# Kernel optimization log

Measured on AMD Instinct MI355X. Metric: run time of the kernel, lower is better.

The kernel has to match this reference:

```python
import jax, jax.numpy as jnp
import numpy as np

B, IN_SEQ, TGT_SEQ = 128, 50, 25
IN_SIZE, OUT_SIZE, RNN = 128, 128, 2048


def setup_inputs() -> dict:
    key = jax.random.key(0)
    ks = jax.random.split(key, 10)
    s_in = 1.0 / np.sqrt(IN_SIZE)
    s_out = 1.0 / np.sqrt(OUT_SIZE)
    s_rnn = 1.0 / np.sqrt(RNN)
    return {
        "encoder_inputs": jax.random.normal(ks[0], (B, IN_SEQ, IN_SIZE), jnp.float32),
        "decoder_inputs": jax.random.normal(ks[1], (B, TGT_SEQ, IN_SIZE), jnp.float32),
        "fc1_w": jax.random.uniform(ks[2], (OUT_SIZE, IN_SIZE), jnp.float32, -s_in, s_in),
        "fc1_b": jax.random.uniform(ks[3], (OUT_SIZE,), jnp.float32, -s_in, s_in),
        "w_ih": jax.random.uniform(ks[4], (3 * RNN, OUT_SIZE), jnp.float32, -s_rnn, s_rnn),
        "w_hh": jax.random.uniform(ks[5], (3 * RNN, RNN), jnp.float32, -s_rnn, s_rnn),
        "b_ih": jax.random.uniform(ks[6], (3 * RNN,), jnp.float32, -s_rnn, s_rnn),
        "b_hh": jax.random.uniform(ks[7], (3 * RNN,), jnp.float32, -s_rnn, s_rnn),
        "fc2_w": jax.random.uniform(ks[8], (OUT_SIZE, RNN), jnp.float32, -s_rnn, s_rnn),
        "fc2_b": jax.random.uniform(ks[9], (OUT_SIZE,), jnp.float32, -s_rnn, s_rnn),
    }


def _gru_cell(x, h, w_ih, w_hh, b_ih, b_hh):
    # PyTorch GRUCell: gates ordered (r, z, n)
    gi = x @ w_ih.T + b_ih            # [B, 3R]
    gh = h @ w_hh.T + b_hh            # [B, 3R]
    i_r, i_z, i_n = jnp.split(gi, 3, axis=-1)
    h_r, h_z, h_n = jnp.split(gh, 3, axis=-1)
    r = jax.nn.sigmoid(i_r + h_r)
    z = jax.nn.sigmoid(i_z + h_z)
    n = jnp.tanh(i_n + r * h_n)
    return (1.0 - z) * n + z * h


def reference(encoder_inputs, decoder_inputs, fc1_w, fc1_b, w_ih, w_hh, b_ih, b_hh, fc2_w, fc2_b):
    # Eval mode: F.dropout(training=False) is identity.
    enc = encoder_inputs @ fc1_w.T + fc1_b              # [B, S_in, OUT]
    enc_t = jnp.transpose(enc, (1, 0, 2))               # time-major [S_in, B, OUT]
    h0 = jnp.zeros((encoder_inputs.shape[0], RNN), enc.dtype)

    def enc_step(state, x):
        return _gru_cell(x, state, w_ih, w_hh, b_ih, b_hh), None

    state, _ = jax.lax.scan(enc_step, h0, enc_t[:-1])   # input_seq - 1 steps

    def dec_step(carry, _):
        state, inp = carry
        inp = jax.lax.stop_gradient(inp)                # inp.detach()
        state = _gru_cell(inp, state, w_ih, w_hh, b_ih, b_hh)
        out = inp + state @ fc2_w.T + fc2_b             # residual decoder
        return (state, out), out

    _, outs = jax.lax.scan(dec_step, (state, enc_t[-1]), None, length=TGT_SEQ)
    return jnp.transpose(outs, (1, 0, 2))               # [B, TGT_SEQ, OUT]
```

## Files before the change

### kernel.cpp

```cpp
#include <hip/hip_runtime.h>
#include <limits.h>

constexpr int kB   = 128;
constexpr int kSin = 50;
constexpr int kT   = 25;
constexpr int kD   = 128;
constexpr int kR   = 2048;
constexpr int kNB  = 256;
constexpr int kNT  = 512;

typedef __bf16 bf16x8 __attribute__((ext_vector_type(8)));
typedef float  f32x4  __attribute__((ext_vector_type(4)));
typedef unsigned short u16;
typedef unsigned long long u64;

__device__ __forceinline__ float bf2f(u16 u){ union{unsigned i; float f;}x; x.i=((unsigned)u)<<16; return x.f; }
__device__ __forceinline__ u16 f2bf(float f){ union{float f; unsigned i;}x; x.f=f; return (u16)((x.i + 0x7FFFu + ((x.i>>16)&1u))>>16); }
__device__ __forceinline__ float sigm(float x){ return 1.f/(1.f+__expf(-x)); }

__device__ __forceinline__ void stg32(unsigned* p, unsigned v){
    __hip_atomic_store(p, v, __ATOMIC_RELAXED, __HIP_MEMORY_SCOPE_AGENT);
}
__device__ __forceinline__ void stg64(u64* p, u64 v){
    __hip_atomic_store(p, v, __ATOMIC_RELAXED, __HIP_MEMORY_SCOPE_AGENT);
}
__device__ __forceinline__ unsigned ald32(const void* p){
    return __hip_atomic_load((const unsigned*)p, __ATOMIC_RELAXED, __HIP_MEMORY_SCOPE_AGENT);
}
__device__ __forceinline__ u64 ald64(const void* p){
    return __hip_atomic_load((const u64*)p, __ATOMIC_RELAXED, __HIP_MEMORY_SCOPE_AGENT);
}
__device__ __forceinline__ bf16x8 ald128bf(const u16* p){
    union{ u64 q[2]; bf16x8 v; } t;
    t.q[0] = ald64(p);
    t.q[1] = ald64(p + 4);
    return t.v;
}
__device__ __forceinline__ float aldf(const float* p){
    union{ unsigned u; float f; } t; t.u = ald32(p); return t.f;
}

__device__ __forceinline__ bf16x8 pack8(float4 a, float4 b){
    union{ bf16x8 v; u16 u[8]; } t;
    t.u[0]=f2bf(a.x); t.u[1]=f2bf(a.y); t.u[2]=f2bf(a.z); t.u[3]=f2bf(a.w);
    t.u[4]=f2bf(b.x); t.u[5]=f2bf(b.y); t.u[6]=f2bf(b.z); t.u[7]=f2bf(b.w);
    return t.v;
}

__device__ __forceinline__ void gbar(int* flags, int k, int base, int perlane)
{
    __syncthreads();
    const int tid = threadIdx.x;
    if (tid == 0) atomicMax(&flags[blockIdx.x*16], k);
    if (tid < 64) {
        int iter = 0;
        for (;;) {
            bool ok = true;
            for (int j = 0; j < perlane; ++j) {
                const int idx = base + tid*perlane + j;
                int v;
                if ((iter & 31) == 31) v = atomicMax(&flags[idx*16], INT_MIN);
                else                   v = (int)ald32(&flags[idx*16]);
                ok &= (v >= k);
            }
            if (__ballot(ok) == ~0ull) break;
            ++iter;
            __builtin_amdgcn_s_sleep(1);
        }
    }
    __syncthreads();
}

__device__ __forceinline__ void cvt_f32_bf16(const float* __restrict__ s, u16* __restrict__ d,
                                             int n4, int gtid, int gstride)
{
    for (int i = gtid; i < n4; i += gstride) {
        float4 v = ((const float4*)s)[i];
        u64 pk = (u64)f2bf(v.x) | ((u64)f2bf(v.y)<<16) | ((u64)f2bf(v.z)<<32) | ((u64)f2bf(v.w)<<48);
        stg64((u64*)d + i, pk);
    }
}

template<int NT, int NACC>
__device__ __forceinline__ void small_gemm(
    const u16* __restrict__ Am, int alda,
    const u16* __restrict__ Bp, int bldb,
    f32x4 (&acc)[NACC], u16* pool)
{
    const int tid=threadIdx.x, lane=tid&63, wv=tid>>6, g=wv>>2, mt=wv&3, ar=lane&15, aq=lane>>4;
    u16* sA = pool;
    u16* sB = pool + 8704;
    { int q=tid,     r=q>>4, c=q&15; *(uint4*)&sA[r*136+c*8] = *(const uint4*)(Am + r*alda + c*8); }
    { int q=tid+512, r=q>>4, c=q&15; *(uint4*)&sA[r*136+c*8] = *(const uint4*)(Am + r*alda + c*8); }
    for (int q=tid; q<NT*256; q+=kNT){
        int r=q>>4, c=q&15;
        *(uint4*)&sB[r*136+c*8] = *(const uint4*)(Bp + (size_t)r*bldb + c*8);
    }
    __syncthreads();
#pragma unroll
    for (int jt=0; jt<NT; ++jt){
        if ((jt&1) != g) continue;
#pragma unroll
        for (int kk=0; kk<4; ++kk){
            bf16x8 a = *(const bf16x8*)&sA[(mt*16+ar)*136 + kk*32 + aq*8];
            bf16x8 b = *(const bf16x8*)&sB[(jt*16+ar)*136 + kk*32 + aq*8];
            acc[jt>>1] = __builtin_amdgcn_mfma_f32_16x16x32_bf16(a,b,acc[jt>>1],0,0,0);
        }
    }
    __syncthreads();
}

__device__ __forceinline__ void gru_phase_reg(
    const u16* __restrict__ hcur, u16* __restrict__ hnxt,
    const u16* __restrict__ xb,
    const bf16x8 (&wB)[3][8], const bf16x8 (&wI)[3],
    const float4 b4, float (&hprev)[4],
    int wgc, int mrow0, u16* smem, u16* sH)
{
    const int tid=threadIdx.x, lane=tid&63, w=tid>>6, ar=lane&15, aq=lane>>4;
    const f32x4 zz = {0.f,0.f,0.f,0.f};
    f32x4 acc[3][4] = {{zz,zz,zz,zz},{zz,zz,zz,zz},{zz,zz,zz,zz}};
    f32x4 xn[4] = {zz,zz,zz,zz};

#pragma unroll
    for (int mt=0; mt<4; ++mt){
        const int row = mrow0 + mt*16 + ar;
        bf16x8 af[8];
#pragma unroll
        for (int c=0; c<8; ++c){
            const int s = 16*w + 2*c + (aq>>1);
            af[c] = ald128bf(hcur + (((s*128 + row)<<4) + (aq&1)*8));
        }
#pragma unroll
        for (int c=0; c<8; ++c){
            acc[0][mt] = __builtin_amdgcn_mfma_f32_16x16x32_bf16(af[c], wB[0][c], acc[0][mt],0,0,0);
            acc[1][mt] = __builtin_amdgcn_mfma_f32_16x16x32_bf16(af[c], wB[1][c], acc[1][mt],0,0,0);
            acc[2][mt] = __builtin_amdgcn_mfma_f32_16x16x32_bf16(af[c], wB[2][c], acc[2][mt],0,0,0);
        }
    }
    if (w < 4){
#pragma unroll
        for (int mt=0; mt<4; ++mt){
            bf16x8 ax = ald128bf(xb + (mrow0+mt*16+ar)*kD + 32*w + aq*8);
            acc[0][mt] = __builtin_amdgcn_mfma_f32_16x16x32_bf16(ax, wI[0], acc[0][mt],0,0,0);
            acc[1][mt] = __builtin_amdgcn_mfma_f32_16x16x32_bf16(ax, wI[1], acc[1][mt],0,0,0);
            xn[mt]     = __builtin_amdgcn_mfma_f32_16x16x32_bf16(ax, wI[2], xn[mt],0,0,0);
        }
    }
    float* red = (float*)smem;
#define RCELL(wp,g4,mt) (red + (((((wp)*4+(g4))*4+(mt))*64 + lane)<<2))
    if (w >= 4){
#pragma unroll
        for (int g=0; g<3; ++g)
#pragma unroll
            for (int mt=0; mt<4; ++mt)
                *(f32x4*)RCELL(w-4, g, mt) = acc[g][mt];
    }
    __syncthreads();
    if (w < 4){
#pragma unroll
        for (int g=0; g<3; ++g)
#pragma unroll
            for (int mt=0; mt<4; ++mt)
                acc[g][mt] += *(f32x4*)RCELL(w, g, mt);
#pragma unroll
        for (int g=0; g<3; ++g)
#pragma unroll
            for (int mt=0; mt<4; ++mt)
                *(f32x4*)RCELL(w, g, mt) = acc[g][mt];
#pragma unroll
        for (int mt=0; mt<4; ++mt)
            *(f32x4*)RCELL(w, 3, mt) = xn[mt];
    }
    __syncthreads();
    if (tid < 256){
        const int mt = tid>>6, ls = tid&63, aqs = ls>>4, ars = ls&15;
        f32x4 R=zz, Z=zz, NH=zz, NX=zz;
#pragma unroll
        for (int wp=0; wp<4; ++wp){
            R  += *(f32x4*)(red + ((((wp*4+0)*4+mt)*64 + ls)<<2));
            Z  += *(f32x4*)(red + ((((wp*4+1)*4+mt)*64 + ls)<<2));
            NH += *(f32x4*)(red + ((((wp*4+2)*4+mt)*64 + ls)<<2));
            NX += *(f32x4*)(red + ((((wp*4+3)*4+mt)*64 + ls)<<2));
        }
#pragma unroll
        for (int rr=0; rr<4; ++rr){
            const int m = mrow0 + mt*16 + aqs*4 + rr;
            float r_ = sigm(R[rr] + b4.x);
            float z_ = sigm(Z[rr] + b4.y);
            float n_ = tanhf(NX[rr] + b4.z + r_*(NH[rr] + b4.w));
            float hn = (1.f-z_)*n_ + z_*hprev[rr];
            hprev[rr] = hn;
            u16 hb = f2bf(hn);
            sH[(mt*16 + aqs*4 + rr)*16 + ars] = hb;
            unsigned other = (unsigned)__shfl_xor((int)(unsigned)hb, 1);
            if (!(ars&1))
                stg32((unsigned*)(hnxt + ((wgc*128+m)<<4) + ars), (unsigned)hb | (other<<16));
        }
    }
#undef RCELL
    __syncthreads();
}

__device__ __forceinline__ void fc2_partial(
    const u16* __restrict__ sH, const bf16x8 (&wF2)[4],
    int wgc, int mh, float* __restrict__ part)
{
    const int tid=threadIdx.x, lane=tid&63, w=tid>>6, ar=lane&15, aq=lane>>4;
    const int mt = w&3, nh = w>>2;
    bf16x8 a;
    if (aq < 2) a = *(const bf16x8*)&sH[(mt*16+ar)*16 + aq*8];
    else {
#pragma unroll
        for (int i=0;i<8;++i) a[i] = (__bf16)0.f;
    }
    const f32x4 zz = {0.f,0.f,0.f,0.f};
    f32x4 acc[4] = {zz,zz,zz,zz};
#pragma unroll
    for (int j=0;j<4;++j)
        acc[j] = __builtin_amdgcn_mfma_f32_16x16x32_bf16(a, wF2[j], acc[j],0,0,0);
#pragma unroll
    for (int j=0;j<4;++j){
        const int col = (nh*4+j)*16 + ar;
#pragma unroll
        for (int rr=0;rr<4;++rr){
            const int row = mt*16 + aq*4 + rr;
            stg32((unsigned*)(part + ((((size_t)mh*64+row)*128 + wgc)*128 + col)),
                  __float_as_uint(acc[j][rr]));
        }
    }
}

__global__ __launch_bounds__(kNT, 2) void seq2seq_kernel(
    const void* __restrict__ enc_in_raw, const void* __restrict__ fc1_w_raw,
    const void* __restrict__ fc1_b_raw,  const void* __restrict__ w_ih_raw,
    const void* __restrict__ w_hh_raw,   const void* __restrict__ b_ih_raw,
    const void* __restrict__ b_hh_raw,   const void* __restrict__ fc2_w_raw,
    const void* __restrict__ fc2_b_raw,
    void* __restrict__ out_raw,
    u16* __restrict__ enc_act,
    u16* __restrict__ h_b16,
    u16* __restrict__ inp_b16,
    float* __restrict__ inp_f32,
    float* __restrict__ encF,
    float* __restrict__ bias,
    float* __restrict__ part,
    int* flags,
    u16* __restrict__ cv_encx, u16* __restrict__ cv_fc2, u16* __restrict__ cv_fc1)
{
    __shared__ __align__(16) u16 smem[33792];
    __shared__ int sflag;
    u16* sH = smem + 32768;
    const int wg = blockIdx.x, tid = threadIdx.x;
    const int wgc = wg & 127, mrow0 = (wg >> 7) * 64;
    const int lane = tid & 63, wv = tid >> 6, ar = lane & 15, aq = lane >> 4;
    const int gtid = wg * kNT + tid, gstride = kNB * kNT;
    const int dom = (wg >> 7) * 128;
    int tok = 1;

    {
        const u16* p = (const u16*)enc_in_raw;
        int found = 0;
        for (int i = tid; i < 16384; i += kNT) found |= ((p[i] & 0x7F80) == 0x7F80) ? 1 : 0;
        if (tid == 0) sflag = 0;
        __syncthreads();
        if (found) sflag = 1;
        __syncthreads();
    }
    const bool F32 = (sflag != 0);

    bf16x8 wB[3][8];
    bf16x8 wI[3];
    {
        const int w4 = wv & 3;
        if (F32){
            const float* Wh = (const float*)w_hh_raw;
            const float* Wi = (const float*)w_ih_raw;
#pragma unroll
            for (int g=0; g<3; ++g)
#pragma unroll
                for (int c=0; c<8; ++c){
                    size_t o = (size_t)(g*kR + wgc*16 + ar)*kR + 256*wv + 32*c + aq*8;
                    wB[g][c] = pack8(*(const float4*)(Wh+o), *(const float4*)(Wh+o+4));
                }
#pragma unroll
            for (int g=0; g<3; ++g){
                size_t o = (size_t)(g*kR + wgc*16 + ar)*kD + 32*w4 + aq*8;
                wI[g] = pack8(*(const float4*)(Wi+o), *(const float4*)(Wi+o+4));
            }
        } else {
            const u16* Wh = (const u16*)w_hh_raw;
            const u16* Wi = (const u16*)w_ih_raw;
#pragma unroll
            for (int g=0; g<3; ++g)
#pragma unroll
                for (int c=0; c<8; ++c)
                    wB[g][c] = *(const bf16x8*)(Wh + (size_t)(g*kR + wgc*16 + ar)*kR + 256*wv + 32*c + aq*8);
#pragma unroll
            for (int g=0; g<3; ++g)
                wI[g] = *(const bf16x8*)(Wi + (size_t)(g*kR + wgc*16 + ar)*kD + 32*w4 + aq*8);
        }
    }

    if (F32) {
        cvt_f32_bf16((const float*)fc2_w_raw, cv_fc2,  (kD*kR)/4,       gtid, gstride);
        cvt_f32_bf16((const float*)fc1_w_raw, cv_fc1,  (kD*kD)/4,       gtid, gstride);
        cvt_f32_bf16((const float*)enc_in_raw,cv_encx, (kB*kSin*kD)/4,  gtid, gstride);
        for (int i = gtid; i < 3*kR; i += gstride) {
            stg32((unsigned*)&bias[i],        __float_as_uint(((const float*)b_ih_raw)[i]));
            stg32((unsigned*)&bias[3*kR + i], __float_as_uint(((const float*)b_hh_raw)[i]));
        }
        for (int i = gtid; i < kD; i += gstride) {
            stg32((unsigned*)&bias[6*kR + i],      __float_as_uint(((const float*)fc1_b_raw)[i]));
            stg32((unsigned*)&bias[6*kR + kD + i], __float_as_uint(((const float*)fc2_b_raw)[i]));
        }
    } else {
        for (int i = gtid; i < 3*kR; i += gstride) {
            stg32((unsigned*)&bias[i],        __float_as_uint(bf2f(((const u16*)b_ih_raw)[i])));
            stg32((unsigned*)&bias[3*kR + i], __float_as_uint(bf2f(((const u16*)b_hh_raw)[i])));
        }
        for (int i = gtid; i < kD; i += gstride) {
            stg32((unsigned*)&bias[6*kR + i],      __float_as_uint(bf2f(((const u16*)fc1_b_raw)[i])));
            stg32((unsigned*)&bias[6*kR + kD + i], __float_as_uint(bf2f(((const u16*)fc2_b_raw)[i])));
        }
    }
    for (int i = gtid; i < (kB*kR)/2; i += gstride) stg32((unsigned*)h_b16 + i, 0u);
    gbar(flags, tok++, 0, 4);

    const u16* ENCX = F32 ? cv_encx : (const u16*)enc_in_raw;
    const u16* WF2  = F32 ? cv_fc2  : (const u16*)fc2_w_raw;
    const u16* WF1  = F32 ? cv_fc1  : (const u16*)fc1_w_raw;

    float4 b4;
    {
        const int hc = wgc*16 + ar;
        b4.x = aldf(&bias[hc])      + aldf(&bias[3*kR+hc]);
        b4.y = aldf(&bias[kR+hc])   + aldf(&bias[4*kR+hc]);
        b4.z = aldf(&bias[2*kR+hc]);
        b4.w = aldf(&bias[5*kR+hc]);
    }
    bf16x8 wF2[4];
    {
        const int nh = wv>>2;
#pragma unroll
        for (int j=0;j<4;++j){
            if (aq < 2)
                wF2[j] = ald128bf(WF2 + (size_t)((nh*4+j)*16+ar)*kR + wgc*16 + aq*8);
            else {
#pragma unroll
                for (int i=0;i<8;++i) wF2[j][i] = (__bf16)0.f;
            }
        }
    }
    const float fc2b = aldf(&bias[6*kR + kD + (wg&1)*64 + (tid&63)]);
    float hprev[4] = {0.f, 0.f, 0.f, 0.f};

    if (wgc < kSin) {
        const int g = wv>>2, mt = wv&3;
        const f32x4 zz = {0.f,0.f,0.f,0.f};
        f32x4 ae[4] = {zz,zz,zz,zz};
        small_gemm<8,4>(ENCX + ((size_t)mrow0*kSin + wgc)*kD, kSin*kD, WF1, kD, ae, smem);
#pragma unroll
        for (int jt=0; jt<8; ++jt){
            if ((jt&1) != g) continue;
            int col = jt*16 + ar;
            float fb = aldf(&bias[6*kR + col]);
#pragma unroll
            for (int rr=0; rr<4; ++rr){
                int m = mrow0 + mt*16 + aq*4 + rr;
                float v = ae[jt>>1][rr] + fb;
                u16 hb = f2bf(v);
                unsigned other = (unsigned)__shfl_xor((int)(unsigned)hb, 1);
                if (!(ar&1))
                    stg32((unsigned*)(enc_act + ((size_t)wgc*kB + m)*kD + col),
                          (unsigned)hb | (other<<16));
                if (wgc == kSin-1)
                    stg32((unsigned*)(encF + (size_t)m*kD + col), __float_as_uint(v));
            }
        }
    }
    gbar(flags, tok++, dom, 2);

    int par = 0;
    for (int t = 0; t < kSin-1; ++t) {
        gru_phase_reg(h_b16 + (size_t)par*kB*kR, h_b16 + (size_t)(1-par)*kB*kR,
                      enc_act + (size_t)t*kB*kD, wB, wI, b4, hprev, wgc, mrow0, smem, sH);
        gbar(flags, tok++, dom, 2);
        par ^= 1;
    }

    const u16*   ib  = enc_act + (size_t)(kSin-1)*kB*kD;
    const float* ifp = encF;
    const int mh = wg >> 7;
    for (int d = 0; d < kT; ++d) {
        gru_phase_reg(h_b16 + (size_t)par*kB*kR, h_b16 + (size_t)(1-par)*kB*kR,
                      ib, wB, wI, b4, hprev, wgc, mrow0, smem, sH);
        fc2_partial(sH, wF2, wgc, mh, part);
        gbar(flags, tok++, dom, 2);
        par ^= 1;

        u16*   nib = inp_b16 + (size_t)(d&1)*kB*kD;
        float* nif = inp_f32 + (size_t)(d&1)*kB*kD;
        {
            const int row = wg >> 1, ch = wg & 1;
            const int mh2 = row >> 6, rl = row & 63;
            const float* pr = part + (size_t)((mh2*64 + rl)*128)*128;
            const int cl = tid & 63, sg = tid >> 6;
            float s = 0.f;
#pragma unroll
            for (int j=0;j<16;++j) s += aldf(&pr[(size_t)(sg*16+j)*128 + ch*64 + cl]);
            float* red2 = (float*)smem;
            red2[sg*64 + cl] = s;
            __syncthreads();
            if (tid < 64){
                float t2 = 0.f;
#pragma unroll
                for (int g2=0; g2<8; ++g2) t2 += red2[g2*64 + tid];
                const int colg = ch*64 + tid;
                const float o = t2 + fc2b + aldf(&ifp[(size_t)row*kD + colg]);
                const size_t ob = ((size_t)row*kT + d)*kD + colg;
                if (F32) ((float*)out_raw)[ob] = o;
                else     ((u16*)out_raw)[ob]   = f2bf(o);
                stg32((unsigned*)(nif + (size_t)row*kD + colg), __float_as_uint(o));
                u16 hb = f2bf(o);
                unsigned other = (unsigned)__shfl_xor((int)(unsigned)hb, 1);
                if (!(tid&1))
                    stg32((unsigned*)(nib + (size_t)row*kD + colg), (unsigned)hb | (other<<16));
            }
        }
        gbar(flags, tok++, dom, 2);
        ib = nib; ifp = nif;
    }
}

extern "C" void kernel_launch(void* const* d_in, const int* in_sizes, int n_in,
                              void* d_out, int out_size, void* d_ws, size_t ws_size,
                              hipStream_t stream)
{
    size_t off = 0;
    char* ws = (char*)d_ws;
    auto alloc = [&](size_t bytes) -> char* {
        char* p = ws + off;
        off = (off + bytes + 255) & ~(size_t)255;
        return p;
    };
    u16*   enc_act = (u16*)alloc((size_t)kSin*kB*kD*2);
    u16*   h_b16   = (u16*)alloc((size_t)2*kB*kR*2);
    u16*   inp_b16 = (u16*)alloc((size_t)2*kB*kD*2);
    float* inp_f32 = (float*)alloc((size_t)2*kB*kD*4);
    float* encF    = (float*)alloc((size_t)kB*kD*4);
    float* bias    = (float*)alloc((size_t)(6*kR + 2*kD)*4);
    float* part    = (float*)alloc((size_t)2*64*128*128*4);
    int*   flags   = (int*)alloc((size_t)kNB*16*4);
    u16*   cv_encx = (u16*)alloc((size_t)kB*kSin*kD*2);
    u16*   cv_fc2  = (u16*)alloc((size_t)kD*kR*2);
    u16*   cv_fc1  = (u16*)alloc((size_t)kD*kD*2);
    (void)ws_size; (void)in_sizes; (void)n_in; (void)out_size;

    seq2seq_kernel<<<dim3(kNB), dim3(kNT), 0, stream>>>(
        d_in[0], d_in[2], d_in[3], d_in[4], d_in[5], d_in[6], d_in[7], d_in[8], d_in[9],
        d_out,
        enc_act, h_b16, inp_b16, inp_f32, encF, bias, part, flags,
        cv_encx, cv_fc2, cv_fc1);
}
```

Baseline: 1.571 ms.

## Replace per-step grid barriers with split arrive and per-wave flag waits

Each GRU recurrence step now replaces the full domain barrier with an arrive (bump own flag) followed by waits at the point of use. Each wave polls only the 16 producer workgroups whose hidden-state slice it reads, and the decoder input is gated by a separate 128-flag wait. This lets waves begin their MFMA work as soon as their own slices are ready, rather than all waiting on the slowest block, and it removes one barrier round-trip. The cost is explicit token bookkeeping, more complex ordering reasoning around the double-buffered hidden state, and polling with s_sleep.

```diff
diff --git a/kernel.cpp b/kernel.cpp
--- a/kernel.cpp
+++ b/kernel.cpp
@@ -45,6 +45,35 @@
     t.u[0]=f2bf(a.x); t.u[1]=f2bf(a.y); t.u[2]=f2bf(a.z); t.u[3]=f2bf(a.w);
     t.u[4]=f2bf(b.x); t.u[5]=f2bf(b.y); t.u[6]=f2bf(b.z); t.u[7]=f2bf(b.w);
     return t.v;
+}
+
+__device__ __forceinline__ int pollflag(int* flags, int idx, int iter){
+    if ((iter & 31) == 31) return atomicMax(&flags[idx*16], INT_MIN);
+    return (int)ald32(&flags[idx*16]);
+}
+__device__ __forceinline__ void wait16(int* flags, int k, int base){
+    const int lane = threadIdx.x & 63;
+    for (int iter = 0;; ++iter){
+        bool ok = true;
+        if (lane < 16) ok = (pollflag(flags, base + lane, iter) >= k);
+        if (__ballot(ok) == ~0ull) return;
+        __builtin_amdgcn_s_sleep(1);
+    }
+}
+__device__ __forceinline__ void wait128(int* flags, int k, int base){
+    const int lane = threadIdx.x & 63;
+    for (int iter = 0;; ++iter){
+        bool ok = true;
+#pragma unroll
+        for (int j = 0; j < 2; ++j)
+            ok &= (pollflag(flags, base + lane*2 + j, iter) >= k);
+        if (__ballot(ok) == ~0ull) return;
+        __builtin_amdgcn_s_sleep(1);
+    }
+}
+__device__ __forceinline__ void arrive(int* flags, int k){
+    __syncthreads();
+    if (threadIdx.x == 0) atomicMax(&flags[blockIdx.x*16], k);
 }
 
 __device__ __forceinline__ void gbar(int* flags, int k, int base, int perlane)
@@ -110,18 +139,21 @@
     __syncthreads();
 }
 
-__device__ __forceinline__ void gru_phase_reg(
+__device__ __forceinline__ void gru_phase_flag(
     const u16* __restrict__ hcur, u16* __restrict__ hnxt,
     const u16* __restrict__ xb,
     const bf16x8 (&wB)[3][8], const bf16x8 (&wI)[3],
     const float4 b4, float (&hprev)[4],
-    int wgc, int mrow0, u16* smem, u16* sH)
+    int wgc, int mrow0, u16* smem, u16* sH,
+    int* flags, int hk, int xk, int fbase)
 {
     const int tid=threadIdx.x, lane=tid&63, w=tid>>6, ar=lane&15, aq=lane>>4;
     const f32x4 zz = {0.f,0.f,0.f,0.f};
     f32x4 acc[3][4] = {{zz,zz,zz,zz},{zz,zz,zz,zz},{zz,zz,zz,zz}};
     f32x4 xn[4] = {zz,zz,zz,zz};
 
+    if (hk) wait16(flags, hk, fbase + 16*w);
+
 #pragma unroll
     for (int mt=0; mt<4; ++mt){
         const int row = mrow0 + mt*16 + ar;
@@ -139,6 +171,7 @@
         }
     }
     if (w < 4){
+        if (xk) wait128(flags, xk, fbase);
 #pragma unroll
         for (int mt=0; mt<4; ++mt){
             bf16x8 ax = ald128bf(xb + (mrow0+mt*16+ar)*kD + 32*w + aq*8);
@@ -256,7 +289,6 @@
     const int lane = tid & 63, wv = tid >> 6, ar = lane & 15, aq = lane >> 4;
     const int gtid = wg * kNT + tid, gstride = kNB * kNT;
     const int dom = (wg >> 7) * 128;
-    int tok = 1;
 
     {
         const u16* p = (const u16*)enc_in_raw;
@@ -325,7 +357,7 @@
         }
     }
     for (int i = gtid; i < (kB*kR)/2; i += gstride) stg32((unsigned*)h_b16 + i, 0u);
-    gbar(flags, tok++, 0, 4);
+    gbar(flags, 1, 0, 4);
 
     const u16* ENCX = F32 ? cv_encx : (const u16*)enc_in_raw;
     const u16* WF2  = F32 ? cv_fc2  : (const u16*)fc2_w_raw;
@@ -379,13 +411,14 @@
             }
         }
     }
-    gbar(flags, tok++, dom, 2);
+    gbar(flags, 2, dom, 2);
 
     int par = 0;
     for (int t = 0; t < kSin-1; ++t) {
-        gru_phase_reg(h_b16 + (size_t)par*kB*kR, h_b16 + (size_t)(1-par)*kB*kR,
-                      enc_act + (size_t)t*kB*kD, wB, wI, b4, hprev, wgc, mrow0, smem, sH);
-        gbar(flags, tok++, dom, 2);
+        gru_phase_flag(h_b16 + (size_t)par*kB*kR, h_b16 + (size_t)(1-par)*kB*kR,
+                       enc_act + (size_t)t*kB*kD, wB, wI, b4, hprev, wgc, mrow0, smem, sH,
+                       flags, (t==0 ? 0 : t+2), 0, dom);
+        arrive(flags, t+3);
         par ^= 1;
     }
 
@@ -393,14 +426,16 @@
     const float* ifp = encF;
     const int mh = wg >> 7;
     for (int d = 0; d < kT; ++d) {
-        gru_phase_reg(h_b16 + (size_t)par*kB*kR, h_b16 + (size_t)(1-par)*kB*kR,
-                      ib, wB, wI, b4, hprev, wgc, mrow0, smem, sH);
+        gru_phase_flag(h_b16 + (size_t)par*kB*kR, h_b16 + (size_t)(1-par)*kB*kR,
+                       ib, wB, wI, b4, hprev, wgc, mrow0, smem, sH,
+                       flags, (d==0 ? 51 : 50+2*d), (d==0 ? 0 : 51+2*d), dom);
         fc2_partial(sH, wF2, wgc, mh, part);
-        gbar(flags, tok++, dom, 2);
+        arrive(flags, 52+2*d);
         par ^= 1;
 
         u16*   nib = inp_b16 + (size_t)(d&1)*kB*kD;
         float* nif = inp_f32 + (size_t)(d&1)*kB*kD;
+        wait128(flags, 52+2*d, dom);
         {
             const int row = wg >> 1, ch = wg & 1;
             const int mh2 = row >> 6, rl = row & 63;
@@ -428,7 +463,7 @@
                     stg32((unsigned*)(nib + (size_t)row*kD + colg), (unsigned)hb | (other<<16));
             }
         }
-        gbar(flags, tok++, dom, 2);
+        arrive(flags, 53+2*d);
         ib = nib; ifp = nif;
     }
 }
```

Result: faster. 1.537 ms (-2.1%).
